# Optimization experiments

Measured on AMD Instinct MI355X. Metric: run time of the kernel, lower is better.

Reference implementation:

```python
import jax, jax.numpy as jnp
import numpy as np

C = 512
C8 = C // 8


def setup_inputs() -> dict:
    key = jax.random.key(0)
    ks = jax.random.split(key, 7)
    B, H, W = 4, 64, 64
    x = jax.random.normal(ks[0], (B, C, H, W), dtype=jnp.float32)
    # 1x1 convs == per-pixel linear maps; store as [C_in, C_out] matrices
    sq = 1.0 / np.sqrt(C)
    wq = jax.random.normal(ks[1], (C, C8), dtype=jnp.float32) * sq
    bq = jnp.zeros((C8,), dtype=jnp.float32)
    wk = jax.random.normal(ks[2], (C, C8), dtype=jnp.float32) * sq
    bk = jnp.zeros((C8,), dtype=jnp.float32)
    wv = jax.random.normal(ks[3], (C, C), dtype=jnp.float32) * sq
    bv = jnp.zeros((C,), dtype=jnp.float32)
    gamma = jnp.zeros((1,), dtype=jnp.float32)  # nn.Parameter(torch.zeros(1))
    return {"x": x, "wq": wq, "bq": bq, "wk": wk, "bk": bk, "wv": wv, "bv": bv, "gamma": gamma}


def reference(x, wq, bq, wk, bk, wv, bv, gamma):
    B, Cc, H, W = x.shape
    N = H * W
    xf = x.reshape(B, Cc, N).transpose(0, 2, 1)          # [B, N, C]
    q = xf @ wq + bq                                     # [B, N, C/8]
    k = xf @ wk + bk                                     # [B, N, C/8]
    v = xf @ wv + bv                                     # [B, N, C]
    energy = jnp.einsum('bnd,bmd->bnm', q, k)            # unscaled QK^T
    attn = jax.nn.softmax(energy, axis=-1)               # [B, N, N]
    out = jnp.einsum('bnm,bmc->bnc', attn, v)            # [B, N, C]
    out = out.transpose(0, 2, 1).reshape(B, Cc, H, W)
    return gamma * out + x
```

## Files before the change

### kernel.cpp

```cpp
#include <hip/hip_runtime.h>

#define BB 4
#define CC 512
#define DD 64
#define NN 4096

__global__ void qkv_or_copy_kernel(const float* __restrict__ x,
                                   const float* __restrict__ wq, const float* __restrict__ bq,
                                   const float* __restrict__ wk, const float* __restrict__ bk,
                                   const float* __restrict__ wv, const float* __restrict__ bv,
                                   const float* __restrict__ gamma,
                                   float* __restrict__ q, float* __restrict__ k,
                                   float* __restrict__ v,
                                   float* __restrict__ out) {
    if (gamma[0] == 0.0f) {
        const float4* __restrict__ x4 = (const float4*)x;
        float4* __restrict__ out4 = (float4*)out;
        const int n4 = (BB * CC * NN) / 4;
        const int stride = gridDim.x * blockDim.x;
        for (int i = blockIdx.x * blockDim.x + threadIdx.x; i < n4; i += stride)
            out4[i] = x4[i];
        return;
    }
    __shared__ float xf[CC];
    const int nrows = BB * NN;
    for (int row = blockIdx.x; row < nrows; row += gridDim.x) {
        const int b = row / NN;
        const int n = row - b * NN;
        for (int c = threadIdx.x; c < CC; c += blockDim.x)
            xf[c] = x[(size_t)b * CC * NN + (size_t)c * NN + n];
        __syncthreads();
        for (int j = threadIdx.x; j < DD + DD + CC; j += blockDim.x) {
            float acc;
            if (j < DD) {
                acc = bq[j];
                for (int c = 0; c < CC; ++c) acc += xf[c] * wq[c * DD + j];
                q[(size_t)row * DD + j] = acc;
            } else if (j < 2 * DD) {
                const int jj = j - DD;
                acc = bk[jj];
                for (int c = 0; c < CC; ++c) acc += xf[c] * wk[c * DD + jj];
                k[(size_t)row * DD + jj] = acc;
            } else {
                const int jj = j - 2 * DD;
                acc = bv[jj];
                for (int c = 0; c < CC; ++c) acc += xf[c] * wv[c * CC + jj];
                v[(size_t)row * CC + jj] = acc;
            }
        }
        __syncthreads();
    }
}

__global__ void attn_kernel(const float* __restrict__ q, const float* __restrict__ k,
                            const float* __restrict__ v, const float* __restrict__ x,
                            const float* __restrict__ gamma,
                            float* __restrict__ out) {
    const float g = gamma[0];
    if (g == 0.0f) return;
    __shared__ float s[NN];
    __shared__ float qrow[DD];
    __shared__ float red[256];
    const int tid = threadIdx.x;
    const int nthr = blockDim.x;
    const int nrows = BB * NN;
    for (int row = blockIdx.x; row < nrows; row += gridDim.x) {
        const int b = row / NN;
        const int n = row - b * NN;
        if (tid < DD) qrow[tid] = q[(size_t)row * DD + tid];
        __syncthreads();
        float lmax = -3.4e38f;
        for (int m = tid; m < NN; m += nthr) {
            const float* kr = &k[((size_t)b * NN + m) * DD];
            float acc = 0.0f;
            for (int d = 0; d < DD; ++d) acc += qrow[d] * kr[d];
            s[m] = acc;
            lmax = fmaxf(lmax, acc);
        }
        red[tid] = lmax;
        __syncthreads();
        for (int off = nthr / 2; off > 0; off >>= 1) {
            if (tid < off) red[tid] = fmaxf(red[tid], red[tid + off]);
            __syncthreads();
        }
        const float m0 = red[0];
        __syncthreads();
        float lsum = 0.0f;
        for (int m = tid; m < NN; m += nthr) {
            const float p = __expf(s[m] - m0);
            s[m] = p;
            lsum += p;
        }
        red[tid] = lsum;
        __syncthreads();
        for (int off = nthr / 2; off > 0; off >>= 1) {
            if (tid < off) red[tid] += red[tid + off];
            __syncthreads();
        }
        const float inv_l = 1.0f / red[0];
        __syncthreads();
        for (int c = tid; c < CC; c += nthr) {
            float acc = 0.0f;
            for (int m = 0; m < NN; ++m)
                acc += s[m] * v[((size_t)b * NN + m) * CC + c];
            const size_t oi = (size_t)b * CC * NN + (size_t)c * NN + n;
            out[oi] = x[oi] + g * acc * inv_l;
        }
        __syncthreads();
    }
}

extern "C" void kernel_launch(void* const* d_in, const int* in_sizes, int n_in,
                              void* d_out, int out_size, void* d_ws, size_t ws_size,
                              hipStream_t stream) {
    const float* x     = (const float*)d_in[0];
    const float* wq    = (const float*)d_in[1];
    const float* bq    = (const float*)d_in[2];
    const float* wk    = (const float*)d_in[3];
    const float* bk    = (const float*)d_in[4];
    const float* wv    = (const float*)d_in[5];
    const float* bv    = (const float*)d_in[6];
    const float* gamma = (const float*)d_in[7];
    float* out = (float*)d_out;

    const size_t qk_elems = (size_t)BB * NN * DD;
    float* q = (float*)d_ws;
    float* k = q + qk_elems;
    float* v = k + qk_elems;

    qkv_or_copy_kernel<<<2048, 256, 0, stream>>>(x, wq, bq, wk, bk, wv, bv,
                                                 gamma, q, k, v, out);
    attn_kernel<<<2048, 256, 0, stream>>>(q, k, v, x, gamma, out);
}
```

Baseline: 17.36 us.

## Fuse QKV projection into attention kernel via reassociated matmuls

Replaces the separate QKV projection kernel and attention kernel with one fused kernel. The key projection is folded into the query (t = Wk·q, so scores come from x·t plus q·bk). The value projection is applied after the attention-weighted sum of x, which avoids materialising K and V in workspace. For the gamma==0 path, this also drops the second, early-returning kernel launch. The trade-off is heavier per-row work and more shared memory when gamma is nonzero.

```diff
diff --git a/kernel.cpp b/kernel.cpp
--- a/kernel.cpp
+++ b/kernel.cpp
@@ -5,15 +5,14 @@
 #define DD 64
 #define NN 4096
 
-__global__ void qkv_or_copy_kernel(const float* __restrict__ x,
-                                   const float* __restrict__ wq, const float* __restrict__ bq,
-                                   const float* __restrict__ wk, const float* __restrict__ bk,
-                                   const float* __restrict__ wv, const float* __restrict__ bv,
-                                   const float* __restrict__ gamma,
-                                   float* __restrict__ q, float* __restrict__ k,
-                                   float* __restrict__ v,
-                                   float* __restrict__ out) {
-    if (gamma[0] == 0.0f) {
+__global__ void attn_fused_kernel(const float* __restrict__ x,
+                                  const float* __restrict__ wq, const float* __restrict__ bq,
+                                  const float* __restrict__ wk, const float* __restrict__ bk,
+                                  const float* __restrict__ wv, const float* __restrict__ bv,
+                                  const float* __restrict__ gamma,
+                                  float* __restrict__ out) {
+    const float g = gamma[0];
+    if (g == 0.0f) {
         const float4* __restrict__ x4 = (const float4*)x;
         float4* __restrict__ out4 = (float4*)out;
         const int n4 = (BB * CC * NN) / 4;
@@ -22,43 +21,10 @@
             out4[i] = x4[i];
         return;
     }
-    __shared__ float xf[CC];
-    const int nrows = BB * NN;
-    for (int row = blockIdx.x; row < nrows; row += gridDim.x) {
-        const int b = row / NN;
-        const int n = row - b * NN;
-        for (int c = threadIdx.x; c < CC; c += blockDim.x)
-            xf[c] = x[(size_t)b * CC * NN + (size_t)c * NN + n];
-        __syncthreads();
-        for (int j = threadIdx.x; j < DD + DD + CC; j += blockDim.x) {
-            float acc;
-            if (j < DD) {
-                acc = bq[j];
-                for (int c = 0; c < CC; ++c) acc += xf[c] * wq[c * DD + j];
-                q[(size_t)row * DD + j] = acc;
-            } else if (j < 2 * DD) {
-                const int jj = j - DD;
-                acc = bk[jj];
-                for (int c = 0; c < CC; ++c) acc += xf[c] * wk[c * DD + jj];
-                k[(size_t)row * DD + jj] = acc;
-            } else {
-                const int jj = j - 2 * DD;
-                acc = bv[jj];
-                for (int c = 0; c < CC; ++c) acc += xf[c] * wv[c * CC + jj];
-                v[(size_t)row * CC + jj] = acc;
-            }
-        }
-        __syncthreads();
-    }
-}
 
-__global__ void attn_kernel(const float* __restrict__ q, const float* __restrict__ k,
-                            const float* __restrict__ v, const float* __restrict__ x,
-                            const float* __restrict__ gamma,
-                            float* __restrict__ out) {
-    const float g = gamma[0];
-    if (g == 0.0f) return;
     __shared__ float s[NN];
+    __shared__ float t[CC];
+    __shared__ float y[CC];
     __shared__ float qrow[DD];
     __shared__ float red[256];
     const int tid = threadIdx.x;
@@ -67,13 +33,28 @@
     for (int row = blockIdx.x; row < nrows; row += gridDim.x) {
         const int b = row / NN;
         const int n = row - b * NN;
-        if (tid < DD) qrow[tid] = q[(size_t)row * DD + tid];
+        const float* __restrict__ xb = x + (size_t)b * CC * NN;
+
+        if (tid < DD) {
+            float acc = bq[tid];
+            for (int c = 0; c < CC; ++c) acc += xb[(size_t)c * NN + n] * wq[c * DD + tid];
+            qrow[tid] = acc;
+        }
         __syncthreads();
+
+        float qb = 0.0f;
+        for (int d = 0; d < DD; ++d) qb += qrow[d] * bk[d];
+        for (int c = tid; c < CC; c += nthr) {
+            float acc = 0.0f;
+            for (int d = 0; d < DD; ++d) acc += wk[c * DD + d] * qrow[d];
+            t[c] = acc;
+        }
+        __syncthreads();
+
         float lmax = -3.4e38f;
         for (int m = tid; m < NN; m += nthr) {
-            const float* kr = &k[((size_t)b * NN + m) * DD];
-            float acc = 0.0f;
-            for (int d = 0; d < DD; ++d) acc += qrow[d] * kr[d];
+            float acc = qb;
+            for (int c = 0; c < CC; ++c) acc += xb[(size_t)c * NN + m] * t[c];
             s[m] = acc;
             lmax = fmaxf(lmax, acc);
         }
@@ -85,6 +66,7 @@
         }
         const float m0 = red[0];
         __syncthreads();
+
         float lsum = 0.0f;
         for (int m = tid; m < NN; m += nthr) {
             const float p = __expf(s[m] - m0);
@@ -99,12 +81,22 @@
         }
         const float inv_l = 1.0f / red[0];
         __syncthreads();
+        for (int m = tid; m < NN; m += nthr) s[m] *= inv_l;
+        __syncthreads();
+
+        for (int cc = tid; cc < CC; cc += nthr) {
+            const float* __restrict__ xr = xb + (size_t)cc * NN;
+            float acc = 0.0f;
+            for (int m = 0; m < NN; ++m) acc += s[m] * xr[m];
+            y[cc] = acc;
+        }
+        __syncthreads();
+
         for (int c = tid; c < CC; c += nthr) {
-            float acc = 0.0f;
-            for (int m = 0; m < NN; ++m)
-                acc += s[m] * v[((size_t)b * NN + m) * CC + c];
+            float acc = bv[c];
+            for (int cc = 0; cc < CC; ++cc) acc += y[cc] * wv[cc * CC + c];
             const size_t oi = (size_t)b * CC * NN + (size_t)c * NN + n;
-            out[oi] = x[oi] + g * acc * inv_l;
+            out[oi] = x[oi] + g * acc;
         }
         __syncthreads();
     }
@@ -123,12 +115,6 @@
     const float* gamma = (const float*)d_in[7];
     float* out = (float*)d_out;
 
-    const size_t qk_elems = (size_t)BB * NN * DD;
-    float* q = (float*)d_ws;
-    float* k = q + qk_elems;
-    float* v = k + qk_elems;
-
-    qkv_or_copy_kernel<<<2048, 256, 0, stream>>>(x, wq, bq, wk, bk, wv, bv,
-                                                 gamma, q, k, v, out);
-    attn_kernel<<<2048, 256, 0, stream>>>(q, k, v, x, gamma, out);
+    attn_fused_kernel<<<2048, 256, 0, stream>>>(x, wq, bq, wk, bk, wv, bv,
+                                                gamma, out);
 }
```

Result: faster. 15.50 us (-10.7%).
